# Optimization experiments

Hardware: AMD Instinct MI355X
Metric: run time of the kernel (lower is better)

## Reference

```python
import jax, jax.numpy as jnp
import numpy as np

SCENE = (128, 128, 16)
NUM_HEADS, NUM_LEVELS, NUM_POINTS = 8, 3, 4
FEAT_SHAPES = ((64, 192), (32, 96), (16, 48))


def _layer_norm(x, g, b, eps=1e-5):
    m = jnp.mean(x, -1, keepdims=True)
    v = jnp.var(x, -1, keepdims=True)
    return (x - m) * jax.lax.rsqrt(v + eps) * g + b


def _bilinear_sample(img, loc):
    # img: [B,H,W,D]; loc in [0,1] coords: [B,N,2] (x,y) -> [B,N,D]
    # matches F.grid_sample(mode='bilinear', padding_mode='zeros', align_corners=False)
    B, H, W, D = img.shape
    x = loc[..., 0] * W - 0.5
    y = loc[..., 1] * H - 0.5
    x0 = jnp.floor(x)
    y0 = jnp.floor(y)
    wx = x - x0
    wy = y - y0
    x0i = x0.astype(jnp.int32)
    y0i = y0.astype(jnp.int32)
    bi = jnp.arange(B)[:, None]

    def tap(ix, iy, w):
        valid = (ix >= 0) & (ix < W) & (iy >= 0) & (iy < H)
        v = img[bi, jnp.clip(iy, 0, H - 1), jnp.clip(ix, 0, W - 1)]
        return v * (w * valid)[..., None]

    return (tap(x0i, y0i, (1 - wx) * (1 - wy)) + tap(x0i + 1, y0i, wx * (1 - wy))
            + tap(x0i, y0i + 1, (1 - wx) * wy) + tap(x0i + 1, y0i + 1, wx * wy))


def _msdeform_attn(query, query_pos, value, ref_pts, Wv, bv, Woff, boff, Wattn, battn, Wout, bout):
    # mmcv MultiScaleDeformableAttention (batch_first), dropout=identity at eval.
    B, Nq, C = query.shape
    Hh, L, P = NUM_HEADS, NUM_LEVELS, NUM_POINTS
    Dh = C // Hh
    identity = query
    q = query + query_pos
    v = (value @ Wv + bv).reshape(B, -1, Hh, Dh)  # [B,S,Hh,Dh]
    off = (q @ Woff + boff).reshape(B, Nq, Hh, L, P, 2)
    aw = jax.nn.softmax((q @ Wattn + battn).reshape(B, Nq, Hh, L * P), axis=-1)
    aw = aw.reshape(B, Nq, Hh, L, P)
    # offset normalizer is (W_l, H_l) per level
    norm = jnp.asarray([[w, h] for (h, w) in FEAT_SHAPES], dtype=q.dtype)  # [L,2]
    loc = ref_pts[:, :, None, None, None, :] + off / norm[None, None, None, :, None, :]
    starts = np.cumsum([0] + [h * w for (h, w) in FEAT_SHAPES])
    acc = jnp.zeros((B * Hh, Nq, Dh), q.dtype)
    for l, (h, w) in enumerate(FEAT_SHAPES):
        img = v[:, starts[l]:starts[l + 1]].reshape(B, h, w, Hh, Dh)
        img = img.transpose(0, 3, 1, 2, 4).reshape(B * Hh, h, w, Dh)
        loc_l = loc[:, :, :, l].transpose(0, 2, 1, 3, 4).reshape(B * Hh, Nq * P, 2)
        sampled = _bilinear_sample(img, loc_l).reshape(B * Hh, Nq, P, Dh)
        w_l = aw[:, :, :, l].transpose(0, 2, 1, 3).reshape(B * Hh, Nq, P)
        acc = acc + jnp.einsum('bnp,bnpd->bnd', w_l, sampled)
    out = acc.reshape(B, Hh, Nq, Dh).transpose(0, 2, 1, 3).reshape(B, Nq, C)
    return identity + out @ Wout + bout


def _forward(scene_embed, scene_pos, ref_pix, feat0, feat1, feat2,
             Wv, bv, Woff, boff, Wattn, battn, Wout, bout, ln_g, ln_b,
             vol_pts, fov_mask):
    bs, V, C = scene_embed.shape
    ncam = fov_mask.shape[1]
    X, Y, Z = SCENE
    # in-bounds voxel mask built by scatter of valid projected points
    keep = ((vol_pts[..., 0] >= 0) & (vol_pts[..., 0] < X)
            & (vol_pts[..., 1] >= 0) & (vol_pts[..., 1] < Y)
            & (vol_pts[..., 2] >= 0) & (vol_pts[..., 2] < Z))
    flat = vol_pts[..., 0] * (Y * Z) + vol_pts[..., 1] * Z + vol_pts[..., 2]
    safe = jnp.where(keep, flat, 0)
    bi = jnp.arange(bs)[:, None]
    pts_mask = (jnp.zeros((bs, V), jnp.int32).at[bi, safe].max(keep.astype(jnp.int32)) > 0)

    # flatten_multi_scale_feats: [B, C, H, W] -> concat over levels of [B, HW, C]
    value = jnp.concatenate(
        [f.reshape(f.shape[0], C, -1).transpose(0, 2, 1) for f in (feat0, feat1, feat2)], axis=1)

    # Padded-equivalent dense dispatch: deformable attention is per-query independent,
    # so running it on ALL voxels per camera and masking on scatter-back is exactly the
    # math of the original ragged gather -> attend -> scatter pipeline.
    S = value.shape[1]
    q = jnp.broadcast_to(scene_embed[:, None], (bs, ncam, V, C)).reshape(bs * ncam, V, C)
    qp = jnp.broadcast_to(scene_pos[:, None], (bs, ncam, V, C)).reshape(bs * ncam, V, C)
    val = jnp.broadcast_to(value[:, None], (bs, ncam, S, C)).reshape(bs * ncam, S, C)
    ref = ref_pix.reshape(bs * ncam, V, 2)
    attn_out = _msdeform_attn(q, qp, val, ref, Wv, bv, Woff, boff, Wattn, battn, Wout, bout)
    attn_out = _layer_norm(attn_out, ln_g, ln_b).reshape(bs, ncam, V, C)

    # scatter back; later cameras overwrite earlier ones (matches python loop order)
    pts_embed = jnp.zeros((bs, V, C), scene_embed.dtype)
    for cam in range(ncam):
        m = (pts_mask & fov_mask[:, cam])[..., None]
        pts_embed = jnp.where(m, attn_out[:, cam], pts_embed)

    x3d = scene_embed.transpose(0, 2, 1)  # nlc_to_nchw then flatten(2): [bs, C, V]
    proposal = jnp.where(pts_mask[:, None, :], pts_embed.transpose(0, 2, 1), x3d)
    return proposal.reshape(bs, C, X, Y, Z)


def setup_inputs():
    key = jax.random.key(0)
    ks = jax.random.split(key, 16)
    C = 128
    X, Y, Z = SCENE
    V = X * Y * Z
    bs, ncam = 1, 1
    f32 = jnp.float32
    Hh, L, P = NUM_HEADS, NUM_LEVELS, NUM_POINTS
    s = 0.02
    vx = jax.random.randint(ks[2], (bs, V), -8, X + 8)
    vy = jax.random.randint(ks[3], (bs, V), -8, Y + 8)
    vz = jax.random.randint(ks[4], (bs, V), -2, Z + 2)
    return {
        'scene_embed': jax.random.normal(ks[0], (bs, V, C), f32),
        'scene_pos': jax.random.normal(ks[1], (bs, V, C), f32),
        'ref_pix': jax.random.uniform(ks[5], (bs, ncam, V, 2), dtype=f32),
        'feat0': jax.random.normal(ks[6], (bs * ncam, C, 64, 192), f32),
        'feat1': jax.random.normal(ks[7], (bs * ncam, C, 32, 96), f32),
        'feat2': jax.random.normal(ks[8], (bs * ncam, C, 16, 48), f32),
        'Wv': jax.random.normal(ks[9], (C, C), f32) * s,
        'bv': jnp.zeros((C,), f32),
        'Woff': jax.random.normal(ks[10], (C, Hh * L * P * 2), f32) * s,
        'boff': jax.random.normal(ks[11], (Hh * L * P * 2,), f32) * s,
        'Wattn': jax.random.normal(ks[12], (C, Hh * L * P), f32) * s,
        'battn': jnp.zeros((Hh * L * P,), f32),
        'Wout': jax.random.normal(ks[13], (C, C), f32) * s,
        'bout': jnp.zeros((C,), f32),
        'ln_g': jnp.ones((C,), f32),
        'ln_b': jnp.zeros((C,), f32),
        'vol_pts': jnp.stack([vx, vy, vz], -1).astype(jnp.int32),
        'fov_mask': jax.random.bernoulli(ks[14], 0.6, (bs, ncam, V)),
    }


def reference(scene_embed, scene_pos, ref_pix, feat0, feat1, feat2,
              Wv, bv, Woff, boff, Wattn, battn, Wout, bout, ln_g, ln_b,
              vol_pts, fov_mask):
    return _forward(scene_embed, scene_pos, ref_pix, feat0, feat1, feat2,
                    Wv, bv, Woff, boff, Wattn, battn, Wout, bout, ln_g, ln_b,
                    vol_pts, fov_mask)
```

## Files before the change

### kernel.cpp

```cpp
#include <hip/hip_runtime.h>


typedef __attribute__((ext_vector_type(8))) short short8v;
typedef __attribute__((ext_vector_type(4))) float f32x4;

#define V_TOT 262144
#define OAS 292
#define NBLK_ATTN 2048

__device__ __forceinline__ unsigned short f2bf(float f) {
  unsigned int u = __float_as_uint(f);
  u += 0x7fffu + ((u >> 16) & 1u);
  return (unsigned short)(u >> 16);
}
__device__ __forceinline__ float bf2f(unsigned short h) {
  return __uint_as_float(((unsigned int)h) << 16);
}

__global__ void zero_kernel(unsigned int* pm) {
  pm[blockIdx.x * 512 + threadIdx.x] = 0u;
}

__global__ void scatter_kernel(const int* __restrict__ vp, unsigned char* __restrict__ pm) {
  int v = blockIdx.x * 512 + threadIdx.x;
  int x = vp[v * 3 + 0], y = vp[v * 3 + 1], z = vp[v * 3 + 2];
  if (x >= 0 && x < 128 && y >= 0 && y < 128 && z >= 0 && z < 16)
    pm[x * 2048 + y * 16 + z] = 1;
}

__global__ void probe_kernel(const unsigned char* __restrict__ fov, int* __restrict__ pflags) {
  int l = threadIdx.x;
  int n = l & 15, kb = (l >> 4) * 8;
  short8v a, b0, b17;
  #pragma unroll
  for (int e = 0; e < 8; ++e) {
    a[e]   = (short)f2bf((float)n);
    b0[e]  = (kb + e == 0)  ? (short)f2bf((float)(n + 1)) : (short)0;
    b17[e] = (kb + e == 17) ? (short)f2bf((float)(n + 3)) : (short)0;
  }
  f32x4 z = {0.f, 0.f, 0.f, 0.f};
  f32x4 d0  = __builtin_amdgcn_mfma_f32_16x16x32_bf16(a, b0,  z, 0, 0, 0);
  f32x4 d17 = __builtin_amdgcn_mfma_f32_16x16x32_bf16(a, b17, z, 0, 0, 0);
  bool ok0 = true, ok1 = true;
  #pragma unroll
  for (int r = 0; r < 4; ++r) {
    float rA = (float)((l >> 4) * 4 + r);
    float cA = (float)(l & 15);
    ok0 = ok0 && (d0[r] == rA * (cA + 1.f)) && (d17[r] == rA * (cA + 3.f));
    ok1 = ok1 && (d0[r] == cA * (rA + 1.f)) && (d17[r] == cA * (rA + 3.f));
  }
  bool all0 = __all(ok0), all1 = __all(ok1);
  if (l == 0) {
    pflags[0] = all0 ? 0 : (all1 ? 1 : 2);
    const unsigned int* fw = (const unsigned int*)fov;
    int i32mode = 1;
    for (int i = 0; i < 8; ++i) i32mode &= (fw[i] <= 1u) ? 1 : 0;
    pflags[1] = i32mode;
  }
}

__global__ void vproj_kernel(const float* __restrict__ f0, const float* __restrict__ f1,
                             const float* __restrict__ f2, const float* __restrict__ Wv,
                             const float* __restrict__ bv, unsigned short* __restrict__ vp) {
  __shared__ __align__(16) float lds[128][20];
  int t = threadIdx.x;
  int s0 = blockIdx.x * 16;
  const float* f; int hw, sl0;
  if (s0 < 12288)      { f = f0; hw = 12288; sl0 = s0; }
  else if (s0 < 15360) { f = f1; hw = 3072;  sl0 = s0 - 12288; }
  else                 { f = f2; hw = 768;   sl0 = s0 - 15360; }
  for (int u = 0; u < 8; ++u) {
    int idx = u * 256 + t;
    int k = idx >> 4, si = idx & 15;
    lds[k][si] = f[(size_t)k * hw + sl0 + si];
  }
  __syncthreads();
  {
    int c = t & 127, half = t >> 7;
    int base = half * 8;
    f32x4 acc0 = {0.f,0.f,0.f,0.f}, acc1 = {0.f,0.f,0.f,0.f};
    #pragma unroll 4
    for (int k = 0; k < 128; ++k) {
      float w = Wv[k * 128 + c];
      f32x4 l0 = *(const f32x4*)&lds[k][base];
      f32x4 l1 = *(const f32x4*)&lds[k][base + 4];
      acc0 += l0 * w;
      acc1 += l1 * w;
    }
    float b = bv[c];
    #pragma unroll
    for (int j = 0; j < 4; ++j) {
      vp[(size_t)(s0 + base + j)     * 128 + c] = f2bf(acc0[j] + b);
      vp[(size_t)(s0 + base + 4 + j) * 128 + c] = f2bf(acc1[j] + b);
    }
  }
}

__global__ void wfrag_kernel(const float* __restrict__ Woff, const float* __restrict__ Wattn,
                             const float* __restrict__ Wout,
                             unsigned short* __restrict__ foa_hi, unsigned short* __restrict__ foa_lo,
                             unsigned short* __restrict__ fout_hi, unsigned short* __restrict__ fout_lo) {
  int t = blockIdx.x * 512 + threadIdx.x;
  int e = t & 7, lane = (t >> 3) & 63, kc = (t >> 9) & 3, nt = t >> 11;
  int k = kc * 32 + (lane >> 4) * 8 + e;
  int j = nt * 16 + (lane & 15);
  float v = (j < 192) ? Woff[k * 192 + j] : ((j < 288) ? Wattn[k * 96 + (j - 192)] : 0.f);
  unsigned short hi = f2bf(v);
  foa_hi[t] = hi;
  foa_lo[t] = f2bf(v - bf2f(hi));
  if (t < 16384) {
    float w = Wout[k * 128 + j];
    unsigned short whi = f2bf(w);
    fout_hi[t] = whi;
    fout_lo[t] = f2bf(w - bf2f(whi));
  }
}

__global__ __launch_bounds__(256) void flagsA_kernel(
    const unsigned char* __restrict__ pmask, const unsigned char* __restrict__ fovmask,
    const int* __restrict__ pflags, unsigned char* __restrict__ flags8,
    unsigned int* __restrict__ blkcnt) {
  __shared__ unsigned int wc[4];
  __shared__ int s_fovint;
  int t = threadIdx.x, b = blockIdx.x;
  int lane = t & 63, wid = t >> 6;
  if (t == 0) s_fovint = pflags[1];
  __syncthreads();
  int v = b * 256 + t;
  int pm = pmask[v];
  int fv = s_fovint ? ((const int*)fovmask)[v] : (int)fovmask[v];
  int fl = pm ? (fv ? 2 : 1) : 0;
  flags8[v] = (unsigned char)fl;
  unsigned long long msk = __ballot(fl == 2);
  if (lane == 0) wc[wid] = (unsigned int)__popcll(msk);
  __syncthreads();
  if (t == 0) blkcnt[b] = wc[0] + wc[1] + wc[2] + wc[3];
}

__global__ __launch_bounds__(1024) void scan_kernel(
    const unsigned int* __restrict__ blkcnt, unsigned int* __restrict__ blkoff,
    unsigned int* __restrict__ counter) {
  __shared__ unsigned int s[1024];
  int t = threadIdx.x;
  unsigned int x = blkcnt[t];
  s[t] = x;
  __syncthreads();
  for (int off = 1; off < 1024; off <<= 1) {
    unsigned int y = (t >= off) ? s[t - off] : 0u;
    __syncthreads();
    s[t] += y;
    __syncthreads();
  }
  blkoff[t] = s[t] - x;
  if (t == 1023) *counter = s[1023];
}

__global__ __launch_bounds__(256) void flagsB_kernel(
    const unsigned char* __restrict__ flags8, const unsigned int* __restrict__ blkoff,
    int* __restrict__ act, int* __restrict__ pidx) {
  __shared__ unsigned int wc[4], wo[4];
  int t = threadIdx.x, b = blockIdx.x;
  int lane = t & 63, wid = t >> 6;
  int v = b * 256 + t;
  int fl = flags8[v];
  unsigned long long msk = __ballot(fl == 2);
  if (lane == 0) wc[wid] = (unsigned int)__popcll(msk);
  __syncthreads();
  if (t == 0) {
    unsigned int s = 0;
    #pragma unroll
    for (int w = 0; w < 4; ++w) { wo[w] = s; s += wc[w]; }
  }
  __syncthreads();
  if (fl == 2) {
    int pos = (int)(blkoff[b] + wo[wid]) + __popcll(msk & ((1ull << lane) - 1ull));
    act[pos] = v;
    pidx[v] = pos;
  }
}

__global__ __launch_bounds__(256) void writer_kernel(
    const float* __restrict__ embed, const unsigned char* __restrict__ flags8,
    const int* __restrict__ pidx, const float* __restrict__ abuf, int mode_buf,
    float* __restrict__ out) {
  __shared__ float tr[64][133];
  __shared__ int sfl[64];
  __shared__ int spx[64];
  int t = threadIdx.x;
  int v0 = blockIdx.x * 64;
  if (t < 64) {
    int fl = flags8[v0 + t];
    sfl[t] = fl;
    spx[t] = (fl == 2) ? pidx[v0 + t] : -1;
  }
  __syncthreads();
  #pragma unroll
  for (int rep = 0; rep < 8; ++rep) {
    int idx = rep * 256 + t;
    int i = idx >> 5, c4 = idx & 31;
    int fl = sfl[i];
    float4 val = {0.f, 0.f, 0.f, 0.f};
    if (mode_buf && fl == 2)
      val = *(const float4*)&abuf[(size_t)spx[i] * 128 + c4 * 4];
    else if (fl == 0)
      val = *(const float4*)&embed[(size_t)(v0 + i) * 128 + c4 * 4];
    tr[i][c4 * 4 + 0] = val.x;
    tr[i][c4 * 4 + 1] = val.y;
    tr[i][c4 * 4 + 2] = val.z;
    tr[i][c4 * 4 + 3] = val.w;
  }
  __syncthreads();
  float4* out4 = (float4*)out;
  #pragma unroll
  for (int rep = 0; rep < 8; ++rep) {
    int task = rep * 256 + t;
    int c = task >> 4, g = task & 15;
    float4 o;
    o.x = tr[g * 4 + 0][c];
    o.y = tr[g * 4 + 1][c];
    o.z = tr[g * 4 + 2][c];
    o.w = tr[g * 4 + 3][c];
    out4[(size_t)c * (V_TOT / 4) + (v0 >> 2) + g] = o;
  }
}

__global__ __launch_bounds__(1024, 4) void attn_kernel(
    const float* __restrict__ embed, const float* __restrict__ pos,
    const float* __restrict__ refp, const unsigned short* __restrict__ vproj,
    const unsigned short* __restrict__ WfragOAh, const unsigned short* __restrict__ WfragOAl,
    const unsigned short* __restrict__ WfragOuth, const unsigned short* __restrict__ WfragOutl,
    const float* __restrict__ boff, const float* __restrict__ battn,
    const float* __restrict__ bout, const float* __restrict__ lng, const float* __restrict__ lnb,
    const int* __restrict__ act, const unsigned int* __restrict__ counter,
    const int* __restrict__ pflags, float* __restrict__ abuf, int dstmode,
    float* __restrict__ out) {
  __shared__ __align__(16) float s_oa[32 * OAS];
  __shared__ __align__(16) unsigned short s_qhi[32 * 128];
  __shared__ __align__(16) unsigned short s_qlo[32 * 128];
  __shared__ int s_vidx[32];
  __shared__ float s_reff[64];
  __shared__ float s_boff[192], s_battn[96], s_bout[128], s_lng[128], s_lnb[128];
  __shared__ int s_meta[3];

  int t = threadIdx.x;
  int wid = t >> 6, lane = t & 63;

  if (t == 0) {
    int cnt = (int)*counter;
    s_meta[0] = cnt;
    s_meta[1] = pflags[0];
    s_meta[2] = (cnt + 31) >> 5;
  }
  if (t < 192) s_boff[t]  = boff[t];
  if (t < 96)  s_battn[t] = battn[t];
  if (t < 128) { s_bout[t] = bout[t]; s_lng[t] = lng[t]; s_lnb[t] = lnb[t]; }
  __syncthreads();
  int count = s_meta[0], mflag = s_meta[1], ntiles = s_meta[2];

  for (int tile = blockIdx.x; tile < ntiles; tile += NBLK_ATTN) {
    int q0 = tile * 32;
    if (t < 32) s_vidx[t] = (q0 + t < count) ? act[q0 + t] : -1;
    if (t < 64) {
      int i = t >> 1, comp = t & 1;
      int idx = q0 + i;
      int vid = (idx < count) ? act[idx] : -1;
      s_reff[t] = (vid >= 0) ? refp[(size_t)vid * 2 + comp] : 0.f;
    }
    {
      int fi = t;
      int i = fi >> 5, c4 = fi & 31;
      int idx = q0 + i;
      int vid = (idx < count) ? act[idx] : -1;
      ushort4 hk = {0,0,0,0}, lk = {0,0,0,0};
      if (vid >= 0) {
        float4 ev = *(const float4*)(embed + (size_t)vid * 128 + c4 * 4);
        float4 pv = *(const float4*)(pos   + (size_t)vid * 128 + c4 * 4);
        float q_0 = ev.x + pv.x, q_1 = ev.y + pv.y, q_2 = ev.z + pv.z, q_3 = ev.w + pv.w;
        hk.x = f2bf(q_0); lk.x = f2bf(q_0 - bf2f(hk.x));
        hk.y = f2bf(q_1); lk.y = f2bf(q_1 - bf2f(hk.y));
        hk.z = f2bf(q_2); lk.z = f2bf(q_2 - bf2f(hk.z));
        hk.w = f2bf(q_3); lk.w = f2bf(q_3 - bf2f(hk.w));
      }
      int c = c4 * 4;
      int idxl = i * 128 + (((c >> 3) ^ (i & 7)) << 3) + (c & 7);
      *(ushort4*)&s_qhi[idxl] = hk;
      *(ushort4*)&s_qlo[idxl] = lk;
    }
    __syncthreads();

    {
      #pragma unroll 1
      for (int tk = wid; tk < 40; tk += 16) {
        int mrow = (tk >= 20) ? 16 : 0;
        int nt = (tk >= 20) ? (tk - 20) : tk;
        f32x4 acc = (f32x4){0.f,0.f,0.f,0.f};
        int arow = mrow + (lane & 15);
        int asub = lane >> 4;
        #pragma unroll 1
        for (int kc = 0; kc < 4; ++kc) {
          int slot = kc * 4 + asub;
          int aidx = arow * 128 + ((slot ^ (arow & 7)) << 3);
          short8v ah = *(const short8v*)&s_qhi[aidx];
          short8v al = *(const short8v*)&s_qlo[aidx];
          size_t bi = (size_t)((nt * 4 + kc) * 64 + lane) * 8;
          short8v bh = *(const short8v*)&WfragOAh[bi];
          short8v bl = *(const short8v*)&WfragOAl[bi];
          acc = __builtin_amdgcn_mfma_f32_16x16x32_bf16(ah, bh, acc, 0, 0, 0);
          acc = __builtin_amdgcn_mfma_f32_16x16x32_bf16(al, bh, acc, 0, 0, 0);
          acc = __builtin_amdgcn_mfma_f32_16x16x32_bf16(ah, bl, acc, 0, 0, 0);
        }
        #pragma unroll
        for (int e = 0; e < 4; ++e) {
          int rr = (mflag == 0) ? ((lane >> 4) * 4 + e) : (lane & 15);
          int cc = (mflag == 0) ? (lane & 15) : ((lane >> 4) * 4 + e);
          int col = nt * 16 + cc;
          if (col < 288) s_oa[(mrow + rr) * OAS + col] = acc[e];
        }
      }
    }
    __syncthreads();

    if (t < 256) {
      int i = t >> 3, h = t & 7;
      float* p = &s_oa[i * OAS + 192 + h * 12];
      const float* bb = &s_battn[h * 12];
      float l[12];
      float m = -1e30f;
      #pragma unroll
      for (int j = 0; j < 12; ++j) { l[j] = p[j] + bb[j]; m = fmaxf(m, l[j]); }
      float sum = 0.f;
      #pragma unroll
      for (int j = 0; j < 12; ++j) { l[j] = __expf(l[j] - m); sum += l[j]; }
      float inv = 1.0f / sum;
      #pragma unroll
      for (int j = 0; j < 12; ++j) p[j] = l[j] * inv;
    }
    __syncthreads();

    {
      const float invWn[3] = {1.f/192.f, 1.f/96.f, 1.f/48.f};
      const float invHn[3] = {1.f/64.f, 1.f/32.f, 1.f/16.f};
      float st[3][3];
      #pragma unroll
      for (int u = 0; u < 3; ++u) {
        int task = u * 1024 + t;
        int i = task / 96, s = task % 96;
        int h = s / 12, lp = s % 12, l = lp >> 2, p = lp & 3;
        int oidx = ((h * 3 + l) * 4 + p) * 2;
        float ox = s_oa[i * OAS + oidx] + s_boff[oidx];
        float oy = s_oa[i * OAS + oidx + 1] + s_boff[oidx + 1];
        float aw = s_oa[i * OAS + 192 + h * 12 + lp];
        st[u][0] = s_reff[i * 2] + ox * invWn[l];
        st[u][1] = s_reff[i * 2 + 1] + oy * invHn[l];
        st[u][2] = aw;
      }
      __syncthreads();
      #pragma unroll
      for (int u = 0; u < 3; ++u) {
        int task = u * 1024 + t;
        int i = task / 96, s = task % 96;
        float* d = &s_oa[i * OAS + s * 3];
        d[0] = st[u][0]; d[1] = st[u][1]; d[2] = st[u][2];
      }
    }
    __syncthreads();

    {
      int i = t >> 5, h = (t >> 2) & 7, q4 = t & 3;
      int dh0 = q4 * 4;
      float acc[4];
      #pragma unroll
      for (int e = 0; e < 4; ++e) acc[e] = 0.f;
      if (s_vidx[i] >= 0) {
        #pragma unroll 2
        for (int lp = 0; lp < 12; ++lp) {
          const int Wl = (lp < 4) ? 192 : ((lp < 8) ? 96 : 48);
          const int Hl = (lp < 4) ? 64 : ((lp < 8) ? 32 : 16);
          const int Bl = (lp < 4) ? 0 : ((lp < 8) ? 12288 : 15360);
          const float* pd = &s_oa[i * OAS + (h * 12 + lp) * 3];
          float lx = pd[0], ly = pd[1], aw = pd[2];
          float x = lx * (float)Wl - 0.5f, y = ly * (float)Hl - 0.5f;
          float xf = floorf(x), yf = floorf(y);
          float wx = x - xf, wy = y - yf;
          int x0 = (int)xf, y0 = (int)yf;
          int x1 = x0 + 1, y1 = y0 + 1;
          int x0c = min(max(x0, 0), Wl - 1), x1c = min(max(x1, 0), Wl - 1);
          int y0c = min(max(y0, 0), Hl - 1), y1c = min(max(y1, 0), Hl - 1);
          float vx0 = (x0 >= 0 && x0 < Wl) ? 1.f : 0.f;
          float vx1 = (x1 >= 0 && x1 < Wl) ? 1.f : 0.f;
          float vy0 = (y0 >= 0 && y0 < Hl) ? 1.f : 0.f;
          float vy1 = (y1 >= 0 && y1 < Hl) ? 1.f : 0.f;
          const unsigned short* vb = vproj + (size_t)Bl * 128 + h * 16 + dh0;
          ushort4 t00 = *(const ushort4*)(vb + (size_t)(y0c * Wl + x0c) * 128);
          ushort4 t01 = *(const ushort4*)(vb + (size_t)(y0c * Wl + x1c) * 128);
          ushort4 t10 = *(const ushort4*)(vb + (size_t)(y1c * Wl + x0c) * 128);
          ushort4 t11 = *(const ushort4*)(vb + (size_t)(y1c * Wl + x1c) * 128);
          float w00 = (1.f - wx) * (1.f - wy) * vx0 * vy0;
          float w01 = wx * (1.f - wy) * vx1 * vy0;
          float w10 = (1.f - wx) * wy * vx0 * vy1;
          float w11 = wx * wy * vx1 * vy1;
          const unsigned short* p00 = (const unsigned short*)&t00;
          const unsigned short* p01 = (const unsigned short*)&t01;
          const unsigned short* p10 = (const unsigned short*)&t10;
          const unsigned short* p11 = (const unsigned short*)&t11;
          #pragma unroll
          for (int e = 0; e < 4; ++e) {
            float sv = w00 * bf2f(p00[e]) + w01 * bf2f(p01[e])
                     + w10 * bf2f(p10[e]) + w11 * bf2f(p11[e]);
            acc[e] += aw * sv;
          }
        }
      }
      int c = h * 16 + dh0;
      int idxl = i * 128 + (((c >> 3) ^ (i & 7)) << 3) + (c & 7);
      ushort4 hk, lk;
      unsigned short* hp = (unsigned short*)&hk;
      unsigned short* lp2 = (unsigned short*)&lk;
      #pragma unroll
      for (int e = 0; e < 4; ++e) {
        unsigned short hi = f2bf(acc[e]);
        hp[e] = hi;
        lp2[e] = f2bf(acc[e] - bf2f(hi));
      }
      *(ushort4*)&s_qhi[idxl] = hk;
      *(ushort4*)&s_qlo[idxl] = lk;
    }
    __syncthreads();

    {
      int mrow = (wid & 1) * 16;
      int nt = wid >> 1;
      f32x4 acc2 = (f32x4){0.f,0.f,0.f,0.f};
      int arow = mrow + (lane & 15);
      int asub = lane >> 4;
      #pragma unroll 1
      for (int kc = 0; kc < 4; ++kc) {
        int slot = kc * 4 + asub;
        int aidx = arow * 128 + ((slot ^ (arow & 7)) << 3);
        short8v ah = *(const short8v*)&s_qhi[aidx];
        short8v al = *(const short8v*)&s_qlo[aidx];
        size_t bi = (size_t)((nt * 4 + kc) * 64 + lane) * 8;
        short8v bh = *(const short8v*)&WfragOuth[bi];
        short8v bl = *(const short8v*)&WfragOutl[bi];
        acc2 = __builtin_amdgcn_mfma_f32_16x16x32_bf16(ah, bh, acc2, 0, 0, 0);
        acc2 = __builtin_amdgcn_mfma_f32_16x16x32_bf16(al, bh, acc2, 0, 0, 0);
        acc2 = __builtin_amdgcn_mfma_f32_16x16x32_bf16(ah, bl, acc2, 0, 0, 0);
      }
      #pragma unroll
      for (int e = 0; e < 4; ++e) {
        int rr = (mflag == 0) ? ((lane >> 4) * 4 + e) : (lane & 15);
        int cc = (mflag == 0) ? (lane & 15) : ((lane >> 4) * 4 + e);
        int row = mrow + rr;
        int col = nt * 16 + cc;
        int vid = s_vidx[row];
        float idv = (vid >= 0) ? embed[(size_t)vid * 128 + col] : 0.f;
        s_oa[row * OAS + col] = acc2[e] + idv + s_bout[col];
      }
    }
    __syncthreads();

    if (t < 512) {
      int i = t >> 4, j = t & 15;
      float* rowp = &s_oa[i * OAS];
      float4 a = *(float4*)&rowp[j * 8];
      float4 b = *(float4*)&rowp[j * 8 + 4];
      float vals[8] = {a.x, a.y, a.z, a.w, b.x, b.y, b.z, b.w};
      float sum = 0.f, sq = 0.f;
      #pragma unroll
      for (int e = 0; e < 8; ++e) { sum += vals[e]; sq += vals[e] * vals[e]; }
      #pragma unroll
      for (int m = 1; m < 16; m <<= 1) {
        sum += __shfl_xor(sum, m);
        sq  += __shfl_xor(sq, m);
      }
      float mean = sum * (1.f / 128.f);
      float var = sq * (1.f / 128.f) - mean * mean;
      float rs = rsqrtf(var + 1e-5f);
      #pragma unroll
      for (int e = 0; e < 8; ++e) {
        int c = j * 8 + e;
        rowp[c] = (vals[e] - mean) * rs * s_lng[c] + s_lnb[c];
      }
    }
    __syncthreads();

    if (dstmode) {
      int i = t >> 5, c4 = t & 31;
      if (s_vidx[i] >= 0) {
        float4 o;
        o.x = s_oa[i * OAS + c4 * 4 + 0];
        o.y = s_oa[i * OAS + c4 * 4 + 1];
        o.z = s_oa[i * OAS + c4 * 4 + 2];
        o.w = s_oa[i * OAS + c4 * 4 + 3];
        *(float4*)&abuf[(size_t)(q0 + i) * 128 + c4 * 4] = o;
      }
    } else {
      #pragma unroll
      for (int rep = 0; rep < 4; ++rep) {
        int idx = rep * 1024 + t;
        int c = idx >> 5, i = idx & 31;
        int vid = s_vidx[i];
        if (vid >= 0) out[(size_t)c * V_TOT + vid] = s_oa[i * OAS + c];
      }
    }
    __syncthreads();
  }
}

extern "C" void kernel_launch(void* const* d_in, const int* in_sizes, int n_in,
                              void* d_out, int out_size, void* d_ws, size_t ws_size,
                              hipStream_t stream) {
  const float* embed = (const float*)d_in[0];
  const float* pos   = (const float*)d_in[1];
  const float* refp  = (const float*)d_in[2];
  const float* f0    = (const float*)d_in[3];
  const float* f1    = (const float*)d_in[4];
  const float* f2    = (const float*)d_in[5];
  const float* Wv    = (const float*)d_in[6];
  const float* bv    = (const float*)d_in[7];
  const float* Woff  = (const float*)d_in[8];
  const float* boff  = (const float*)d_in[9];
  const float* Wattn = (const float*)d_in[10];
  const float* battn = (const float*)d_in[11];
  const float* Wout  = (const float*)d_in[12];
  const float* bout  = (const float*)d_in[13];
  const float* lng   = (const float*)d_in[14];
  const float* lnb   = (const float*)d_in[15];
  const int*   volp  = (const int*)d_in[16];
  const unsigned char* fov = (const unsigned char*)d_in[17];
  float* out = (float*)d_out;

  char* ws = (char*)d_ws;
  unsigned short* vproj  = (unsigned short*)(ws + 0);
  unsigned char*  pmask  = (unsigned char*)(ws + 4128768);
  unsigned int*   counter= (unsigned int*)(ws + 4390912);
  int*            pflags = (int*)(ws + 4391040);
  unsigned short* foa_hi = (unsigned short*)(ws + 4391168);
  unsigned short* foa_lo = (unsigned short*)(ws + 4473088);
  unsigned short* fout_hi= (unsigned short*)(ws + 4555008);
  unsigned short* fout_lo= (unsigned short*)(ws + 4587776);
  int*            act    = (int*)(ws + 4833536);
  unsigned char*  flags8 = (unsigned char*)(ws + 5882112);
  int*            pidx   = (int*)(ws + 6144256);
  unsigned int*   blkcnt = (unsigned int*)(ws + 7192832);
  unsigned int*   blkoff = (unsigned int*)(ws + 7196928);
  float*          abuf   = (float*)(ws + 7201024);

  int use_buf = (ws_size >= (size_t)7201024 + (size_t)134217728) ? 1 : 0;

  zero_kernel<<<128, 512, 0, stream>>>((unsigned int*)pmask);
  scatter_kernel<<<512, 512, 0, stream>>>(volp, pmask);
  probe_kernel<<<1, 64, 0, stream>>>(fov, pflags);
  vproj_kernel<<<1008, 256, 0, stream>>>(f0, f1, f2, Wv, bv, vproj);
  wfrag_kernel<<<80, 512, 0, stream>>>(Woff, Wattn, Wout, foa_hi, foa_lo,
                                       fout_hi, fout_lo);
  flagsA_kernel<<<1024, 256, 0, stream>>>(pmask, fov, pflags, flags8, blkcnt);
  scan_kernel<<<1, 1024, 0, stream>>>(blkcnt, blkoff, counter);
  flagsB_kernel<<<1024, 256, 0, stream>>>(flags8, blkoff, act, pidx);

  if (use_buf) {
    attn_kernel<<<NBLK_ATTN, 1024, 0, stream>>>(embed, pos, refp, vproj,
                                                foa_hi, foa_lo, fout_hi, fout_lo,
                                                boff, battn, bout, lng, lnb,
                                                act, counter, pflags, abuf, 1, out);
    writer_kernel<<<4096, 256, 0, stream>>>(embed, flags8, pidx, abuf, 1, out);
  } else {
    writer_kernel<<<4096, 256, 0, stream>>>(embed, flags8, pidx, abuf, 0, out);
    attn_kernel<<<NBLK_ATTN, 1024, 0, stream>>>(embed, pos, refp, vproj,
                                                foa_hi, foa_lo, fout_hi, fout_lo,
                                                boff, battn, bout, lng, lnb,
                                                act, counter, pflags, abuf, 0, out);
  }
}
```

Baseline: 306.3 us.

## Split sampling points across lanes with full-head vector loads and shuffle reduction

Each group of four lanes now handles one query-head pair by splitting its twelve sampling points three per lane, instead of splitting the 16 head channels four per lane. Every lane loads all 16 channels of each bilinear tap as two 16-byte vector loads, and the four partial sums are combined with xor shuffles. This divides the per-lane location and weight arithmetic by four and issues fewer, wider gathers. In exchange each lane holds 16 accumulators, and acc[g*4+e] is indexed by lane at runtime, which may push that array into scratch memory and add register pressure.

```diff
diff --git a/kernel.cpp b/kernel.cpp
--- a/kernel.cpp
+++ b/kernel.cpp
@@ -2,6 +2,7 @@
 
 
 typedef __attribute__((ext_vector_type(8))) short short8v;
+typedef __attribute__((ext_vector_type(8))) unsigned short u16x8;
 typedef __attribute__((ext_vector_type(4))) float f32x4;
 
 #define V_TOT 262144
@@ -366,17 +367,18 @@
     __syncthreads();
 
     {
-      int i = t >> 5, h = (t >> 2) & 7, q4 = t & 3;
-      int dh0 = q4 * 4;
-      float acc[4];
-      #pragma unroll
-      for (int e = 0; e < 4; ++e) acc[e] = 0.f;
+      int qh = t >> 2, g = t & 3;
+      int i = qh >> 3, h = qh & 7;
+      float acc[16];
+      #pragma unroll
+      for (int e = 0; e < 16; ++e) acc[e] = 0.f;
       if (s_vidx[i] >= 0) {
-        #pragma unroll 2
-        for (int lp = 0; lp < 12; ++lp) {
-          const int Wl = (lp < 4) ? 192 : ((lp < 8) ? 96 : 48);
-          const int Hl = (lp < 4) ? 64 : ((lp < 8) ? 32 : 16);
-          const int Bl = (lp < 4) ? 0 : ((lp < 8) ? 12288 : 15360);
+        #pragma unroll 1
+        for (int sub = 0; sub < 3; ++sub) {
+          int lp = g * 3 + sub;
+          int l = lp >> 2;
+          int Wl = 192 >> l, Hl = 64 >> l;
+          int Bl = (l == 0) ? 0 : ((l == 1) ? 12288 : 15360);
           const float* pd = &s_oa[i * OAS + (h * 12 + lp) * 3];
           float lx = pd[0], ly = pd[1], aw = pd[2];
           float x = lx * (float)Wl - 0.5f, y = ly * (float)Hl - 0.5f;
@@ -390,37 +392,57 @@
           float vx1 = (x1 >= 0 && x1 < Wl) ? 1.f : 0.f;
           float vy0 = (y0 >= 0 && y0 < Hl) ? 1.f : 0.f;
           float vy1 = (y1 >= 0 && y1 < Hl) ? 1.f : 0.f;
-          const unsigned short* vb = vproj + (size_t)Bl * 128 + h * 16 + dh0;
-          ushort4 t00 = *(const ushort4*)(vb + (size_t)(y0c * Wl + x0c) * 128);
-          ushort4 t01 = *(const ushort4*)(vb + (size_t)(y0c * Wl + x1c) * 128);
-          ushort4 t10 = *(const ushort4*)(vb + (size_t)(y1c * Wl + x0c) * 128);
-          ushort4 t11 = *(const ushort4*)(vb + (size_t)(y1c * Wl + x1c) * 128);
           float w00 = (1.f - wx) * (1.f - wy) * vx0 * vy0;
           float w01 = wx * (1.f - wy) * vx1 * vy0;
           float w10 = (1.f - wx) * wy * vx0 * vy1;
           float w11 = wx * wy * vx1 * vy1;
-          const unsigned short* p00 = (const unsigned short*)&t00;
-          const unsigned short* p01 = (const unsigned short*)&t01;
-          const unsigned short* p10 = (const unsigned short*)&t10;
-          const unsigned short* p11 = (const unsigned short*)&t11;
-          #pragma unroll
-          for (int e = 0; e < 4; ++e) {
-            float sv = w00 * bf2f(p00[e]) + w01 * bf2f(p01[e])
-                     + w10 * bf2f(p10[e]) + w11 * bf2f(p11[e]);
-            acc[e] += aw * sv;
+          const unsigned short* vb = vproj + (size_t)Bl * 128 + h * 16;
+          int o00 = (y0c * Wl + x0c) << 7;
+          int o01 = (y0c * Wl + x1c) << 7;
+          int o10 = (y1c * Wl + x0c) << 7;
+          int o11 = (y1c * Wl + x1c) << 7;
+          {
+            u16x8 t00 = *(const u16x8*)(vb + o00);
+            u16x8 t01 = *(const u16x8*)(vb + o01);
+            u16x8 t10 = *(const u16x8*)(vb + o10);
+            u16x8 t11 = *(const u16x8*)(vb + o11);
+            #pragma unroll
+            for (int e = 0; e < 8; ++e) {
+              float sv = w00 * bf2f(t00[e]) + w01 * bf2f(t01[e])
+                       + w10 * bf2f(t10[e]) + w11 * bf2f(t11[e]);
+              acc[e] += aw * sv;
+            }
+          }
+          {
+            u16x8 t00 = *(const u16x8*)(vb + o00 + 8);
+            u16x8 t01 = *(const u16x8*)(vb + o01 + 8);
+            u16x8 t10 = *(const u16x8*)(vb + o10 + 8);
+            u16x8 t11 = *(const u16x8*)(vb + o11 + 8);
+            #pragma unroll
+            for (int e = 0; e < 8; ++e) {
+              float sv = w00 * bf2f(t00[e]) + w01 * bf2f(t01[e])
+                       + w10 * bf2f(t10[e]) + w11 * bf2f(t11[e]);
+              acc[8 + e] += aw * sv;
+            }
           }
         }
       }
-      int c = h * 16 + dh0;
+      #pragma unroll
+      for (int e = 0; e < 16; ++e) {
+        acc[e] += __shfl_xor(acc[e], 1);
+        acc[e] += __shfl_xor(acc[e], 2);
+      }
+      int c = h * 16 + g * 4;
       int idxl = i * 128 + (((c >> 3) ^ (i & 7)) << 3) + (c & 7);
       ushort4 hk, lk;
       unsigned short* hp = (unsigned short*)&hk;
       unsigned short* lp2 = (unsigned short*)&lk;
       #pragma unroll
       for (int e = 0; e < 4; ++e) {
-        unsigned short hi = f2bf(acc[e]);
+        float v = acc[g * 4 + e];
+        unsigned short hi = f2bf(v);
         hp[e] = hi;
-        lp2[e] = f2bf(acc[e] - bf2f(hi));
+        lp2[e] = f2bf(v - bf2f(hi));
       }
       *(ushort4*)&s_qhi[idxl] = hk;
       *(ushort4*)&s_qlo[idxl] = lk;
```

New measurement: 466.2 us. 52.2% more time.
